# Kernel optimization log

Measured on AMD Instinct MI355X. Metric: run time of the kernel, lower is better.

The kernel has to match this reference:

```python
import jax, jax.numpy as jnp
import numpy as np

NUM_USER = 100000
NUM_ITEM = 50000
N = NUM_USER + NUM_ITEM
E = 1200000
D = 64          # emb_size
F_ITEM = 384    # raw item multimodal feature dim
K = 3           # number of global embedding rows (summed over dim 0)
N_LAYERS = 4
EPS = 1e-8      # F.cosine_similarity default eps


def setup_inputs() -> dict:
    key = jax.random.key(0)
    ks = jax.random.split(key, 9)
    return {
        "adj_row": jax.random.randint(ks[0], (E,), 0, N),
        "adj_col": jax.random.randint(ks[1], (E,), 0, N),
        # scaled like a degree-normalized adjacency (avg degree ~8)
        "adj_val": jax.random.uniform(ks[2], (E,), jnp.float32) / 8.0,
        "user_fea": jax.random.normal(ks[3], (NUM_USER, D), jnp.float32) * 0.1,
        "item_fea": jax.random.normal(ks[4], (NUM_ITEM, F_ITEM), jnp.float32) * 0.1,
        "g_emb_u": jax.random.normal(ks[5], (K, D), jnp.float32) * 0.1,
        "g_emb_i": jax.random.normal(ks[6], (K, D), jnp.float32) * 0.1,
        "mlp_w": jax.random.normal(ks[7], (D, F_ITEM), jnp.float32) * (1.0 / np.sqrt(F_ITEM)),
        "mlp_b": jnp.zeros((D,), jnp.float32),
    }


def _cosine_sim(a, b):
    # matches F.cosine_similarity(a, b, dim=-1) with eps clamp on norms
    na = jnp.maximum(jnp.linalg.norm(a, axis=-1), EPS)
    nb = jnp.maximum(jnp.linalg.norm(b, axis=-1), EPS)
    return jnp.sum(a * b, axis=-1) / (na * nb)


def reference(adj_row, adj_col, adj_val, user_fea, item_fea, g_emb_u, g_emb_i, mlp_w, mlp_b):
    # global embeddings summed over modality dim
    user_emb = user_fea + jnp.sum(g_emb_u, axis=0)                       # [U, D]
    item_emb = jnp.tanh(item_fea @ mlp_w.T + mlp_b) + jnp.sum(g_emb_i, axis=0)  # [I, D]
    ego = jnp.concatenate([user_emb, item_emb], axis=0)                  # [N, D]

    x = ego
    acc = ego  # sum over layers, includes layer-0 (ego) term
    for _ in range(N_LAYERS):
        # sparse adj @ x as gather -> scale -> segment-sum scatter
        x = jax.ops.segment_sum(adj_val[:, None] * x[adj_col], adj_row, num_segments=N)
        w = _cosine_sim(x, ego)     # [N]
        x = w[:, None] * x          # einsum('a,ab->ab')
        acc = acc + x

    return acc[:NUM_USER], acc[NUM_USER:]
```

## Files before the change

kernel.cpp:

```cpp
#include <hip/hip_runtime.h>
#include <hip/hip_bf16.h>

#define U_NUM 100000
#define I_NUM 50000
#define N_NUM 150000
#define E_NUM 1200000
#define D 64
#define F_IT 384
#define CAP 32
#define EPSV 1e-8f
#define FXS 524288.0f
#define FXI (1.0f / 524288.0f)

typedef unsigned short ushort_t;
typedef unsigned int uint_t;
typedef short bf16x8 __attribute__((ext_vector_type(8)));
typedef float f32x4 __attribute__((ext_vector_type(4)));

__device__ __forceinline__ ushort_t f2bf(float f) {
    uint_t x = __float_as_uint(f);
    uint_t r = x + 0x7fffu + ((x >> 16) & 1u);
    return (ushort_t)(r >> 16);
}
__device__ __forceinline__ float bfu2f(uint_t u_lo16) {
    return __uint_as_float(u_lo16 << 16);
}
__device__ __forceinline__ void dec8(uint4 u, float* f) {
    f[0] = bfu2f(u.x & 0xffffu); f[1] = bfu2f(u.x >> 16);
    f[2] = bfu2f(u.y & 0xffffu); f[3] = bfu2f(u.y >> 16);
    f[4] = bfu2f(u.z & 0xffffu); f[5] = bfu2f(u.z >> 16);
    f[6] = bfu2f(u.w & 0xffffu); f[7] = bfu2f(u.w >> 16);
}

__global__ void k_prep(const float* __restrict__ w, const float* __restrict__ gu,
                       const float* __restrict__ gi,
                       int* __restrict__ cnt, short* __restrict__ wbf,
                       float* __restrict__ gsu, float* __restrict__ gsi) {
    int b = blockIdx.x, t = threadIdx.x;
    if (b < 586) {
        int i = b * 256 + t;
        if (i < N_NUM) cnt[i] = 0;
    } else if (b < 682) {
        int i = (b - 586) * 256 + t;
        wbf[i] = (short)f2bf(w[i]);
    } else {
        if (t < 64) gsu[t] = gu[t] + gu[64 + t] + gu[128 + t];
        else if (t < 128) { int d = t - 64; gsi[d] = gi[d] + gi[64 + d] + gi[128 + d]; }
    }
}

#define FILL_B 1172
#define ITEM_B 782
#define USER_B 1563

__global__ __launch_bounds__(256) void k_mega(
        const int* __restrict__ row, const int* __restrict__ col,
        const float* __restrict__ val,
        const float* __restrict__ ufea, const float* __restrict__ ifea,
        const float* __restrict__ bvec,
        const short* __restrict__ wbf,
        const float* __restrict__ gsu, const float* __restrict__ gsi,
        int* __restrict__ cnt, int2* __restrict__ bkt,
        float* __restrict__ ego, ushort_t* __restrict__ egob) {
    int b = blockIdx.x;
    int grp = b / 9, slot = b % 9;
    int tid = threadIdx.x;

    if (slot < 3) {
        int fid = grp * 3 + slot;
        if (fid >= FILL_B) return;
        int t = fid * 256 + tid;
        if (t >= E_NUM / 4) return;
        int r[4], c[4];
        float v[4];
#pragma unroll
        for (int k = 0; k < 4; k++) {
            int e = t + k * (E_NUM / 4);
            r[k] = row[e]; c[k] = col[e]; v[k] = val[e];
        }
        int p[4];
#pragma unroll
        for (int k = 0; k < 4; k++) p[k] = atomicAdd(&cnt[r[k]], 1);
#pragma unroll
        for (int k = 0; k < 4; k++) {
            if (p[k] < CAP) bkt[r[k] * CAP + p[k]] = make_int2(c[k], __float_as_int(v[k]));
        }
    } else if (slot < 5) {
        int iid = grp * 2 + (slot - 3);
        if (iid >= ITEM_B) return;
        int wave = tid >> 6, lane = tid & 63;
        int q = lane >> 4, m = lane & 15;
        int ibase = iid * 64 + wave * 16;
        int irow = min(ibase + m, I_NUM - 1);
        const float* arow = ifea + (size_t)irow * F_IT + q * 8;

        f32x4 av[4];
#pragma unroll
        for (int n = 0; n < 4; n++) av[n] = (f32x4){0.f, 0.f, 0.f, 0.f};
#pragma unroll
        for (int c = 0; c < 12; c++) {
            float4 fa0 = ((const float4*)(arow + c * 32))[0];
            float4 fa1 = ((const float4*)(arow + c * 32))[1];
            bf16x8 af;
            af[0] = (short)f2bf(fa0.x); af[1] = (short)f2bf(fa0.y);
            af[2] = (short)f2bf(fa0.z); af[3] = (short)f2bf(fa0.w);
            af[4] = (short)f2bf(fa1.x); af[5] = (short)f2bf(fa1.y);
            af[6] = (short)f2bf(fa1.z); af[7] = (short)f2bf(fa1.w);
#pragma unroll
            for (int n = 0; n < 4; n++) {
                bf16x8 bf = *(const bf16x8*)(wbf + (size_t)(n * 16 + m) * F_IT + c * 32 + q * 8);
                av[n] = __builtin_amdgcn_mfma_f32_16x16x32_bf16(af, bf, av[n], 0, 0, 0);
            }
        }
#pragma unroll
        for (int n = 0; n < 4; n++) {
            int dim = n * 16 + m;
            float bb = bvec[dim];
            float gg = gsi[dim];
#pragma unroll
            for (int rr = 0; rr < 4; rr++) {
                int item = ibase + q * 4 + rr;
                if (item < I_NUM) {
                    float v = tanhf(av[n][rr] + bb) + gg;
                    size_t o = (size_t)(U_NUM + item) * D + dim;
                    ego[o] = v;
                    egob[o] = f2bf(v);
                }
            }
        }
    } else {
        int uid = grp * 4 + (slot - 5);
        if (uid >= USER_B) return;
        int t = uid * 256 + tid;
        size_t base = (size_t)t * 16;
        if (base >= (size_t)U_NUM * D) return;
        int d0 = (int)(base & 63);
        float f[16];
#pragma unroll
        for (int k = 0; k < 4; k++) {
            float4 v = ((const float4*)(ufea + base))[k];
            f[4 * k] = v.x; f[4 * k + 1] = v.y; f[4 * k + 2] = v.z; f[4 * k + 3] = v.w;
        }
#pragma unroll
        for (int j = 0; j < 16; j++) f[j] += gsu[d0 + j];
#pragma unroll
        for (int k = 0; k < 4; k++) {
            ((float4*)(ego + base))[k] = make_float4(f[4 * k], f[4 * k + 1], f[4 * k + 2], f[4 * k + 3]);
        }
        uint4 u0, u1;
        u0.x = (uint_t)f2bf(f[0]) | ((uint_t)f2bf(f[1]) << 16);
        u0.y = (uint_t)f2bf(f[2]) | ((uint_t)f2bf(f[3]) << 16);
        u0.z = (uint_t)f2bf(f[4]) | ((uint_t)f2bf(f[5]) << 16);
        u0.w = (uint_t)f2bf(f[6]) | ((uint_t)f2bf(f[7]) << 16);
        u1.x = (uint_t)f2bf(f[8]) | ((uint_t)f2bf(f[9]) << 16);
        u1.y = (uint_t)f2bf(f[10]) | ((uint_t)f2bf(f[11]) << 16);
        u1.z = (uint_t)f2bf(f[12]) | ((uint_t)f2bf(f[13]) << 16);
        u1.w = (uint_t)f2bf(f[14]) | ((uint_t)f2bf(f[15]) << 16);
        ((uint4*)(egob + base))[0] = u0;
        ((uint4*)(egob + base))[1] = u1;
    }
}

#define ACC8(A, VS, X) \
    A[0] += __float2int_rn(VS * bfu2f(X.x & 0xffffu)); A[1] += __float2int_rn(VS * bfu2f(X.x >> 16)); \
    A[2] += __float2int_rn(VS * bfu2f(X.y & 0xffffu)); A[3] += __float2int_rn(VS * bfu2f(X.y >> 16)); \
    A[4] += __float2int_rn(VS * bfu2f(X.z & 0xffffu)); A[5] += __float2int_rn(VS * bfu2f(X.z >> 16)); \
    A[6] += __float2int_rn(VS * bfu2f(X.w & 0xffffu)); A[7] += __float2int_rn(VS * bfu2f(X.w >> 16));

__device__ __forceinline__ float row_weight(const float* a, const float* e) {
    float dot = 0.f, nx = 0.f, ne = 0.f;
#pragma unroll
    for (int j = 0; j < 8; j++) {
        dot += a[j] * e[j]; nx += a[j] * a[j]; ne += e[j] * e[j];
    }
#pragma unroll
    for (int m = 1; m < 8; m <<= 1) {
        dot += __shfl_xor(dot, m);
        nx  += __shfl_xor(nx, m);
        ne  += __shfl_xor(ne, m);
    }
    return dot / (fmaxf(sqrtf(nx), EPSV) * fmaxf(sqrtf(ne), EPSV));
}

__global__ __launch_bounds__(256) void k_spmm(const ushort_t* __restrict__ xb,
                                              const ushort_t* __restrict__ egob,
                                              const int* __restrict__ cnt,
                                              const int2* __restrict__ bkt,
                                              ushort_t* __restrict__ xob) {
    int t = blockIdx.x * 256 + threadIdx.x;
    int l = t & 7, g = t >> 3;
    if (g >= N_NUM / 2) return;
    int r0 = g * 2, r1 = r0 + 1;
    int deg0 = min(cnt[r0], CAP), deg1 = min(cnt[r1], CAP);
    const int2* bp0 = bkt + (size_t)r0 * CAP;
    const int2* bp1 = bkt + (size_t)r1 * CAP;
    int2 p0[4] = {bp0[l], bp0[l + 8], bp0[l + 16], bp0[l + 24]};
    int2 p1[4] = {bp1[l], bp1[l + 8], bp1[l + 16], bp1[l + 24]};
    int a0[8], a1[8];
#pragma unroll
    for (int j = 0; j < 8; j++) { a0[j] = 0; a1[j] = 0; }
    int dmax = max(deg0, deg1);
#pragma unroll
    for (int k = 0; k < 4; k++) {
        if (k * 8 < dmax) {
            int c0x = p0[k].x, c0y = p0[k].y, c1x = p1[k].x, c1y = p1[k].y;
#pragma unroll
            for (int j = 0; j < 8; j++) {
                int cc0 = __shfl(c0x, j, 8);
                float v0 = __int_as_float(__shfl(c0y, j, 8));
                if ((k * 8 + j) >= deg0) { cc0 = 0; v0 = 0.f; }
                uint4 xv = ((const uint4*)xb)[(size_t)cc0 * 8 + l];
                int cc1 = __shfl(c1x, j, 8);
                float v1 = __int_as_float(__shfl(c1y, j, 8));
                if ((k * 8 + j) >= deg1) { cc1 = 0; v1 = 0.f; }
                uint4 yv = ((const uint4*)xb)[(size_t)cc1 * 8 + l];
                float vs0 = v0 * FXS, vs1 = v1 * FXS;
                ACC8(a0, vs0, xv);
                ACC8(a1, vs1, yv);
            }
        }
    }
#pragma unroll
    for (int rr = 0; rr < 2; rr++) {
        int r = rr ? r1 : r0;
        const int* ai = rr ? a1 : a0;
        float a[8];
#pragma unroll
        for (int j = 0; j < 8; j++) a[j] = (float)ai[j] * FXI;
        float e[8]; dec8(((const uint4*)egob)[(size_t)r * 8 + l], e);
        float wgt = row_weight(a, e);
        uint4 ov;
        ov.x = (uint_t)f2bf(wgt * a[0]) | ((uint_t)f2bf(wgt * a[1]) << 16);
        ov.y = (uint_t)f2bf(wgt * a[2]) | ((uint_t)f2bf(wgt * a[3]) << 16);
        ov.z = (uint_t)f2bf(wgt * a[4]) | ((uint_t)f2bf(wgt * a[5]) << 16);
        ov.w = (uint_t)f2bf(wgt * a[6]) | ((uint_t)f2bf(wgt * a[7]) << 16);
        ((uint4*)xob)[(size_t)r * 8 + l] = ov;
    }
}

__global__ __launch_bounds__(256) void k_spmm4(const ushort_t* __restrict__ x3,
                                               const ushort_t* __restrict__ x1,
                                               const ushort_t* __restrict__ x2,
                                               const float* __restrict__ ego,
                                               const int* __restrict__ cnt,
                                               const int2* __restrict__ bkt,
                                               float* __restrict__ out) {
    int t = blockIdx.x * 256 + threadIdx.x;
    int l = t & 7, g = t >> 3;
    if (g >= N_NUM / 2) return;
    int r0 = g * 2, r1 = r0 + 1;
    int deg0 = min(cnt[r0], CAP), deg1 = min(cnt[r1], CAP);
    const int2* bp0 = bkt + (size_t)r0 * CAP;
    const int2* bp1 = bkt + (size_t)r1 * CAP;
    int2 p0[4] = {bp0[l], bp0[l + 8], bp0[l + 16], bp0[l + 24]};
    int2 p1[4] = {bp1[l], bp1[l + 8], bp1[l + 16], bp1[l + 24]};
    int a0[8], a1[8];
#pragma unroll
    for (int j = 0; j < 8; j++) { a0[j] = 0; a1[j] = 0; }
    int dmax = max(deg0, deg1);
#pragma unroll
    for (int k = 0; k < 4; k++) {
        if (k * 8 < dmax) {
            int c0x = p0[k].x, c0y = p0[k].y, c1x = p1[k].x, c1y = p1[k].y;
#pragma unroll
            for (int j = 0; j < 8; j++) {
                int cc0 = __shfl(c0x, j, 8);
                float v0 = __int_as_float(__shfl(c0y, j, 8));
                if ((k * 8 + j) >= deg0) { cc0 = 0; v0 = 0.f; }
                uint4 xv = ((const uint4*)x3)[(size_t)cc0 * 8 + l];
                int cc1 = __shfl(c1x, j, 8);
                float v1 = __int_as_float(__shfl(c1y, j, 8));
                if ((k * 8 + j) >= deg1) { cc1 = 0; v1 = 0.f; }
                uint4 yv = ((const uint4*)x3)[(size_t)cc1 * 8 + l];
                float vs0 = v0 * FXS, vs1 = v1 * FXS;
                ACC8(a0, vs0, xv);
                ACC8(a1, vs1, yv);
            }
        }
    }
#pragma unroll
    for (int rr = 0; rr < 2; rr++) {
        int r = rr ? r1 : r0;
        const int* ai = rr ? a1 : a0;
        float a[8];
#pragma unroll
        for (int j = 0; j < 8; j++) a[j] = (float)ai[j] * FXI;
        size_t rb = (size_t)r * D + l * 8;
        float e[8];
        float4 e0 = ((const float4*)(ego + rb))[0];
        float4 e1 = ((const float4*)(ego + rb))[1];
        e[0] = e0.x; e[1] = e0.y; e[2] = e0.z; e[3] = e0.w;
        e[4] = e1.x; e[5] = e1.y; e[6] = e1.z; e[7] = e1.w;
        float wgt = row_weight(a, e);
        float s[8];
        float x1d[8], x2d[8], x3d[8];
        dec8(((const uint4*)x1)[(size_t)r * 8 + l], x1d);
        dec8(((const uint4*)x2)[(size_t)r * 8 + l], x2d);
        dec8(((const uint4*)x3)[(size_t)r * 8 + l], x3d);
#pragma unroll
        for (int j = 0; j < 8; j++) s[j] = e[j] + x1d[j] + x2d[j] + x3d[j] + wgt * a[j];
        ((float4*)(out + rb))[0] = make_float4(s[0], s[1], s[2], s[3]);
        ((float4*)(out + rb))[1] = make_float4(s[4], s[5], s[6], s[7]);
    }
}

extern "C" void kernel_launch(void* const* d_in, const int* in_sizes, int n_in,
                              void* d_out, int out_size, void* d_ws, size_t ws_size,
                              hipStream_t stream) {
    const int*   adj_row  = (const int*)d_in[0];
    const int*   adj_col  = (const int*)d_in[1];
    const float* adj_val  = (const float*)d_in[2];
    const float* user_fea = (const float*)d_in[3];
    const float* item_fea = (const float*)d_in[4];
    const float* gu       = (const float*)d_in[5];
    const float* gi       = (const float*)d_in[6];
    const float* mlp_w    = (const float*)d_in[7];
    const float* mlp_b    = (const float*)d_in[8];

    float* out = (float*)d_out;

    char* ws = (char*)d_ws;
    size_t off = 0;
    float*    ego  = (float*)(ws + off);    off += (size_t)N_NUM * D * 4;
    ushort_t* egob = (ushort_t*)(ws + off); off += (size_t)N_NUM * D * 2;
    ushort_t* x1   = (ushort_t*)(ws + off); off += (size_t)N_NUM * D * 2;
    ushort_t* x2   = (ushort_t*)(ws + off); off += (size_t)N_NUM * D * 2;
    ushort_t* x3   = (ushort_t*)(ws + off); off += (size_t)N_NUM * D * 2;
    int*      cnt  = (int*)(ws + off);      off += (size_t)N_NUM * 4;
    short*    wbf  = (short*)(ws + off);    off += (size_t)D * F_IT * 2;
    float*    gsu  = (float*)(ws + off);    off += 64 * 4;
    float*    gsi  = (float*)(ws + off);    off += 64 * 4;
    off = (off + 255) & ~(size_t)255;
    int2*     bkt  = (int2*)(ws + off);     off += (size_t)N_NUM * CAP * 8;

    k_prep<<<683, 256, 0, stream>>>(mlp_w, gu, gi, cnt, wbf, gsu, gsi);
    k_mega<<<391 * 9, 256, 0, stream>>>(adj_row, adj_col, adj_val, user_fea, item_fea,
                                        mlp_b, wbf, gsu, gsi, cnt, bkt, ego, egob);
    int g = (N_NUM / 2 * 8 + 255) / 256;
    k_spmm<<<g, 256, 0, stream>>>(egob, egob, cnt, bkt, x1);
    k_spmm<<<g, 256, 0, stream>>>(x1,   egob, cnt, bkt, x2);
    k_spmm<<<g, 256, 0, stream>>>(x2,   egob, cnt, bkt, x3);
    k_spmm4<<<g, 256, 0, stream>>>(x3, x1, x2, ego, cnt, bkt, out);
}
```

Measured before the change: 412.6 us.

## Build CSR buckets via two-pass binned partition instead of global atomics

Replaces the single-pass global-atomic bucket fill with a two-stage scheme. First, each fill block partitions its edges into 586 row bins using shared-memory atomics, writing to per-block cells that reuse the x1 buffer, with a small overflow area. Then a new k_bucket kernel scatters each bin's edges into per-row slots using shared-memory counters. The goal is to remove contended global atomics and scattered writes at the cost of an extra kernel launch, plus data loss if a cell and its overflow both fill. The spmm kernels also now prefetch the next 8 bucket entries instead of loading all 32 up front, which lowers register pressure and avoids loads past the row degree.

```diff
diff --git a/kernel.cpp b/kernel.cpp
--- a/kernel.cpp
+++ b/kernel.cpp
@@ -12,6 +12,12 @@
 #define FXS 524288.0f
 #define FXI (1.0f / 524288.0f)
 
+#define NBIN 586
+#define RPB 256
+#define FBLK 586
+#define CELL_CAP 16
+#define OV_CAP 64
+
 typedef unsigned short ushort_t;
 typedef unsigned int uint_t;
 typedef short bf16x8 __attribute__((ext_vector_type(8)));
@@ -34,22 +40,19 @@
 
 __global__ void k_prep(const float* __restrict__ w, const float* __restrict__ gu,
                        const float* __restrict__ gi,
-                       int* __restrict__ cnt, short* __restrict__ wbf,
-                       float* __restrict__ gsu, float* __restrict__ gsi) {
+                       short* __restrict__ wbf, float* __restrict__ gsu,
+                       float* __restrict__ gsi, int* __restrict__ ovcnt) {
     int b = blockIdx.x, t = threadIdx.x;
-    if (b < 586) {
+    if (b < 96) {
         int i = b * 256 + t;
-        if (i < N_NUM) cnt[i] = 0;
-    } else if (b < 682) {
-        int i = (b - 586) * 256 + t;
         wbf[i] = (short)f2bf(w[i]);
     } else {
         if (t < 64) gsu[t] = gu[t] + gu[64 + t] + gu[128 + t];
         else if (t < 128) { int d = t - 64; gsi[d] = gi[d] + gi[64 + d] + gi[128 + d]; }
-    }
-}
-
-#define FILL_B 1172
+        for (int i = t; i < NBIN; i += 256) ovcnt[i] = 0;
+    }
+}
+
 #define ITEM_B 782
 #define USER_B 1563
 
@@ -60,33 +63,43 @@
         const float* __restrict__ bvec,
         const short* __restrict__ wbf,
         const float* __restrict__ gsu, const float* __restrict__ gsi,
-        int* __restrict__ cnt, int2* __restrict__ bkt,
+        int2* __restrict__ cellbuf, int* __restrict__ cellcnt,
+        int* __restrict__ ovcnt, int2* __restrict__ ovbuf,
         float* __restrict__ ego, ushort_t* __restrict__ egob) {
+    __shared__ int bincnt[NBIN];
     int b = blockIdx.x;
     int grp = b / 9, slot = b % 9;
     int tid = threadIdx.x;
 
-    if (slot < 3) {
-        int fid = grp * 3 + slot;
-        if (fid >= FILL_B) return;
+    if (slot < 2) {
+        int fid = grp * 2 + slot;
+        if (fid >= FBLK) return;
+        for (int i = tid; i < NBIN; i += 256) bincnt[i] = 0;
+        __syncthreads();
         int t = fid * 256 + tid;
-        if (t >= E_NUM / 4) return;
-        int r[4], c[4];
-        float v[4];
-#pragma unroll
-        for (int k = 0; k < 4; k++) {
-            int e = t + k * (E_NUM / 4);
-            r[k] = row[e]; c[k] = col[e]; v[k] = val[e];
-        }
-        int p[4];
-#pragma unroll
-        for (int k = 0; k < 4; k++) p[k] = atomicAdd(&cnt[r[k]], 1);
-#pragma unroll
-        for (int k = 0; k < 4; k++) {
-            if (p[k] < CAP) bkt[r[k] * CAP + p[k]] = make_int2(c[k], __float_as_int(v[k]));
-        }
-    } else if (slot < 5) {
-        int iid = grp * 2 + (slot - 3);
+        if (t < E_NUM / 8) {
+#pragma unroll
+            for (int k = 0; k < 8; k++) {
+                int e = k * (E_NUM / 8) + t;
+                int r = row[e], c = col[e];
+                float v = val[e];
+                int bn = r >> 8;
+                int key = c | ((r & 255) << 18);
+                int ls = atomicAdd(&bincnt[bn], 1);
+                if (ls < CELL_CAP) {
+                    cellbuf[((size_t)fid * NBIN + bn) * CELL_CAP + ls] =
+                        make_int2(key, __float_as_int(v));
+                } else {
+                    int o = atomicAdd(&ovcnt[bn], 1);
+                    if (o < OV_CAP) ovbuf[bn * OV_CAP + o] = make_int2(key, __float_as_int(v));
+                }
+            }
+        }
+        __syncthreads();
+        for (int i = tid; i < NBIN; i += 256)
+            cellcnt[(size_t)fid * NBIN + i] = min(bincnt[i], CELL_CAP);
+    } else if (slot < 4) {
+        int iid = grp * 2 + (slot - 2);
         if (iid >= ITEM_B) return;
         int wave = tid >> 6, lane = tid & 63;
         int q = lane >> 4, m = lane & 15;
@@ -129,7 +142,7 @@
             }
         }
     } else {
-        int uid = grp * 4 + (slot - 5);
+        int uid = grp * 5 + (slot - 4);
         if (uid >= USER_B) return;
         int t = uid * 256 + tid;
         size_t base = (size_t)t * 16;
@@ -159,6 +172,45 @@
         ((uint4*)(egob + base))[0] = u0;
         ((uint4*)(egob + base))[1] = u1;
     }
+}
+
+__global__ __launch_bounds__(256) void k_bucket(const int2* __restrict__ cellbuf,
+                                                const int* __restrict__ cellcnt,
+                                                const int* __restrict__ ovcnt,
+                                                const int2* __restrict__ ovbuf,
+                                                int* __restrict__ cnt,
+                                                int2* __restrict__ bkt) {
+    __shared__ int lc[RPB];
+    int bn = blockIdx.x, tid = threadIdx.x;
+    lc[tid] = 0;
+    __syncthreads();
+    int rbase = bn << 8;
+    int f0 = tid, f1 = tid + 256, f2 = tid + 512;
+    int c0 = cellcnt[(size_t)f0 * NBIN + bn];
+    int c1 = cellcnt[(size_t)f1 * NBIN + bn];
+    int c2 = (f2 < FBLK) ? cellcnt[(size_t)f2 * NBIN + bn] : 0;
+#pragma unroll
+    for (int h = 0; h < 3; h++) {
+        int f = (h == 0) ? f0 : ((h == 1) ? f1 : f2);
+        int c = (h == 0) ? c0 : ((h == 1) ? c1 : c2);
+        const int2* cp = cellbuf + ((size_t)f * NBIN + bn) * CELL_CAP;
+        for (int i = 0; i < c; i++) {
+            int2 e = cp[i];
+            int rl = e.x >> 18;
+            int s = atomicAdd(&lc[rl], 1);
+            if (s < CAP) bkt[(size_t)(rbase + rl) * CAP + s] = make_int2(e.x & 0x3ffff, e.y);
+        }
+    }
+    int oc = min(ovcnt[bn], OV_CAP);
+    for (int i = tid; i < oc; i += 256) {
+        int2 e = ovbuf[bn * OV_CAP + i];
+        int rl = e.x >> 18;
+        int s = atomicAdd(&lc[rl], 1);
+        if (s < CAP) bkt[(size_t)(rbase + rl) * CAP + s] = make_int2(e.x & 0x3ffff, e.y);
+    }
+    __syncthreads();
+    int r = rbase + tid;
+    if (r < N_NUM) cnt[r] = lc[tid];
 }
 
 #define ACC8(A, VS, X) \
@@ -194,16 +246,18 @@
     int deg0 = min(cnt[r0], CAP), deg1 = min(cnt[r1], CAP);
     const int2* bp0 = bkt + (size_t)r0 * CAP;
     const int2* bp1 = bkt + (size_t)r1 * CAP;
-    int2 p0[4] = {bp0[l], bp0[l + 8], bp0[l + 16], bp0[l + 24]};
-    int2 p1[4] = {bp1[l], bp1[l + 8], bp1[l + 16], bp1[l + 24]};
+    int dmax = max(deg0, deg1);
+    int2 pc0 = bp0[l], pc1 = bp1[l];
     int a0[8], a1[8];
 #pragma unroll
     for (int j = 0; j < 8; j++) { a0[j] = 0; a1[j] = 0; }
-    int dmax = max(deg0, deg1);
 #pragma unroll
     for (int k = 0; k < 4; k++) {
         if (k * 8 < dmax) {
-            int c0x = p0[k].x, c0y = p0[k].y, c1x = p1[k].x, c1y = p1[k].y;
+            bool nn = (k < 3) && ((k + 1) * 8 < dmax);
+            int2 n0 = make_int2(0, 0), n1 = make_int2(0, 0);
+            if (nn) { n0 = bp0[l + (k + 1) * 8]; n1 = bp1[l + (k + 1) * 8]; }
+            int c0x = pc0.x, c0y = pc0.y, c1x = pc1.x, c1y = pc1.y;
 #pragma unroll
             for (int j = 0; j < 8; j++) {
                 int cc0 = __shfl(c0x, j, 8);
@@ -218,6 +272,7 @@
                 ACC8(a0, vs0, xv);
                 ACC8(a1, vs1, yv);
             }
+            if (nn) { pc0 = n0; pc1 = n1; }
         }
     }
 #pragma unroll
@@ -252,16 +307,18 @@
     int deg0 = min(cnt[r0], CAP), deg1 = min(cnt[r1], CAP);
     const int2* bp0 = bkt + (size_t)r0 * CAP;
     const int2* bp1 = bkt + (size_t)r1 * CAP;
-    int2 p0[4] = {bp0[l], bp0[l + 8], bp0[l + 16], bp0[l + 24]};
-    int2 p1[4] = {bp1[l], bp1[l + 8], bp1[l + 16], bp1[l + 24]};
+    int dmax = max(deg0, deg1);
+    int2 pc0 = bp0[l], pc1 = bp1[l];
     int a0[8], a1[8];
 #pragma unroll
     for (int j = 0; j < 8; j++) { a0[j] = 0; a1[j] = 0; }
-    int dmax = max(deg0, deg1);
 #pragma unroll
     for (int k = 0; k < 4; k++) {
         if (k * 8 < dmax) {
-            int c0x = p0[k].x, c0y = p0[k].y, c1x = p1[k].x, c1y = p1[k].y;
+            bool nn = (k < 3) && ((k + 1) * 8 < dmax);
+            int2 n0 = make_int2(0, 0), n1 = make_int2(0, 0);
+            if (nn) { n0 = bp0[l + (k + 1) * 8]; n1 = bp1[l + (k + 1) * 8]; }
+            int c0x = pc0.x, c0y = pc0.y, c1x = pc1.x, c1y = pc1.y;
 #pragma unroll
             for (int j = 0; j < 8; j++) {
                 int cc0 = __shfl(c0x, j, 8);
@@ -276,6 +333,7 @@
                 ACC8(a0, vs0, xv);
                 ACC8(a1, vs1, yv);
             }
+            if (nn) { pc0 = n0; pc1 = n1; }
         }
     }
 #pragma unroll
@@ -323,6 +381,7 @@
     size_t off = 0;
     float*    ego  = (float*)(ws + off);    off += (size_t)N_NUM * D * 4;
     ushort_t* egob = (ushort_t*)(ws + off); off += (size_t)N_NUM * D * 2;
+    size_t x1off = off;
     ushort_t* x1   = (ushort_t*)(ws + off); off += (size_t)N_NUM * D * 2;
     ushort_t* x2   = (ushort_t*)(ws + off); off += (size_t)N_NUM * D * 2;
     ushort_t* x3   = (ushort_t*)(ws + off); off += (size_t)N_NUM * D * 2;
@@ -332,10 +391,16 @@
     float*    gsi  = (float*)(ws + off);    off += 64 * 4;
     off = (off + 255) & ~(size_t)255;
     int2*     bkt  = (int2*)(ws + off);     off += (size_t)N_NUM * CAP * 8;
-
-    k_prep<<<683, 256, 0, stream>>>(mlp_w, gu, gi, cnt, wbf, gsu, gsi);
+    int*      cellcnt = (int*)(ws + off);   off += (size_t)FBLK * NBIN * 4;
+    int*      ovcnt   = (int*)(ws + off);   off += (size_t)NBIN * 4;
+    int2*     ovbuf   = (int2*)(ws + off);  off += (size_t)NBIN * OV_CAP * 8;
+    int2*     cellbuf = (int2*)(ws + x1off);
+
+    k_prep<<<97, 256, 0, stream>>>(mlp_w, gu, gi, wbf, gsu, gsi, ovcnt);
     k_mega<<<391 * 9, 256, 0, stream>>>(adj_row, adj_col, adj_val, user_fea, item_fea,
-                                        mlp_b, wbf, gsu, gsi, cnt, bkt, ego, egob);
+                                        mlp_b, wbf, gsu, gsi,
+                                        cellbuf, cellcnt, ovcnt, ovbuf, ego, egob);
+    k_bucket<<<NBIN, 256, 0, stream>>>(cellbuf, cellcnt, ovcnt, ovbuf, cnt, bkt);
     int g = (N_NUM / 2 * 8 + 255) / 256;
     k_spmm<<<g, 256, 0, stream>>>(egob, egob, cnt, bkt, x1);
     k_spmm<<<g, 256, 0, stream>>>(x1,   egob, cnt, bkt, x2);
```

After: 422.6 us. 1.02x slower.
